# Optimization experiments

Hardware: AMD Instinct MI355X
Metric: run time of the kernel (lower is better)

Reference implementation:

```python
import jax, jax.numpy as jnp
import numpy as np

D_MODEL = 256
HEADS = 4
HEAD_DIM = D_MODEL // HEADS  # 64
BN_EPS = 1e-5


def conv1(x, W, b):
    # Conv1d kernel_size=1 == per-position linear: x [B,C,N], W [O,C], b [O]
    return jnp.einsum('oc,bcn->bon', W, x) + b[:, None]


def setup_inputs() -> dict:
    key = jax.random.key(0)
    ks = jax.random.split(key, 12)
    B, N, M = 4, 4096, 4096
    s = 0.02
    return {
        'x': jax.random.normal(ks[0], (B, D_MODEL, N), jnp.float32),
        'source': jax.random.normal(ks[1], (B, D_MODEL, M), jnp.float32),
        'pq_w': jax.random.normal(ks[2], (D_MODEL, D_MODEL), jnp.float32) * s,
        'pq_b': jnp.zeros((D_MODEL,), jnp.float32),
        'pk_w': jax.random.normal(ks[3], (D_MODEL, D_MODEL), jnp.float32) * s,
        'pk_b': jnp.zeros((D_MODEL,), jnp.float32),
        'pv_w': jax.random.normal(ks[4], (D_MODEL, D_MODEL), jnp.float32) * s,
        'pv_b': jnp.zeros((D_MODEL,), jnp.float32),
        'merge_w': jax.random.normal(ks[5], (D_MODEL, D_MODEL), jnp.float32) * s,
        'merge_b': jnp.zeros((D_MODEL,), jnp.float32),
        'mlp1_w': jax.random.normal(ks[6], (2 * D_MODEL, 2 * D_MODEL), jnp.float32) * s,
        'mlp1_b': jax.random.normal(ks[7], (2 * D_MODEL,), jnp.float32) * s,
        'bn_gamma': jnp.ones((2 * D_MODEL,), jnp.float32),
        'bn_beta': jnp.zeros((2 * D_MODEL,), jnp.float32),
        'mlp2_w': jax.random.normal(ks[8], (D_MODEL, 2 * D_MODEL), jnp.float32) * s,
        'mlp2_b': jnp.zeros((D_MODEL,), jnp.float32),  # nn.init.constant_(mlp[-1].bias, 0.0)
    }


def reference(x, source, pq_w, pq_b, pk_w, pk_b, pv_w, pv_b,
              merge_w, merge_b, mlp1_w, mlp1_b, bn_gamma, bn_beta,
              mlp2_w, mlp2_b):
    B = x.shape[0]
    # projections; torch view(B, dim, heads, -1): channels split as (head_dim, heads)
    q = conv1(x, pq_w, pq_b).reshape(B, HEAD_DIM, HEADS, -1)       # [B,d,h,N]
    k = conv1(source, pk_w, pk_b).reshape(B, HEAD_DIM, HEADS, -1)  # [B,d,h,M]
    v = conv1(source, pv_w, pv_b).reshape(B, HEAD_DIM, HEADS, -1)
    scores = jnp.einsum('bdhn,bdhm->bhnm', q, k) / (HEAD_DIM ** 0.5)
    prob = jax.nn.softmax(scores, axis=-1)                          # [B,h,N,M]
    attn_out = jnp.einsum('bhnm,bdhm->bdhn', prob, v).reshape(B, D_MODEL, -1)
    message = conv1(attn_out, merge_w, merge_b)                     # [B,D,N]
    # MLP: conv(512->512) + BatchNorm1d (training-mode batch stats) + ReLU + conv(512->256)
    h = conv1(jnp.concatenate([x, message], axis=1), mlp1_w, mlp1_b)  # [B,2D,N]
    mean = jnp.mean(h, axis=(0, 2), keepdims=True)
    var = jnp.var(h, axis=(0, 2), keepdims=True)  # biased, as torch BN uses for normalization
    h = bn_gamma[:, None] * (h - mean) * jax.lax.rsqrt(var + BN_EPS) + bn_beta[:, None]
    h = jax.nn.relu(h)
    return conv1(h, mlp2_w, mlp2_b)
```

## Files before the change

kernel.cpp:

```cpp
#include <hip/hip_runtime.h>
#include <hip/hip_bf16.h>

#define D_MODEL 256
#define HEADS 4
#define HD 64
#define BATCH 4
#define SEQ 4096
#define NPOS (BATCH*SEQ)
#define SCALE_LOG2 0.18033688011112042f
#define MCHUNKS 2

typedef __attribute__((ext_vector_type(4))) float floatx4;
typedef __attribute__((ext_vector_type(8))) short bf16x8;
typedef __attribute__((ext_vector_type(4))) short bf16x4;
typedef __attribute__((ext_vector_type(4))) unsigned short ushortx4;

__device__ __forceinline__ float bf2f(unsigned short b) {
    return __uint_as_float(((unsigned int)b) << 16);
}
__device__ __forceinline__ unsigned short f2bf(float f) {
    unsigned int u = __float_as_uint(f);
    return (unsigned short)((u + 0x7fffu + ((u >> 16) & 1u)) >> 16);
}
__device__ __forceinline__ bf16x4 pack_bf16x4(float a, float b, float c, float d) {
    __hip_bfloat162 lo = __float22bfloat162_rn(float2{a, b});
    __hip_bfloat162 hi = __float22bfloat162_rn(float2{c, d});
    union { __hip_bfloat162 h2[2]; bf16x4 v; } u;
    u.h2[0] = lo; u.h2[1] = hi;
    return u.v;
}
__device__ __forceinline__ bf16x8 pack_bf16x8(floatx4 a, floatx4 b) {
    union { bf16x4 h[2]; bf16x8 v; } u;
    u.h[0] = pack_bf16x4(a[0], a[1], a[2], a[3]);
    u.h[1] = pack_bf16x4(b[0], b[1], b[2], b[3]);
    return u.v;
}
#define MFMA(a,b,c) __builtin_amdgcn_mfma_f32_16x16x32_bf16((a),(b),(c),0,0,0)
#define EXP2(x) __builtin_amdgcn_exp2f(x)

__global__ __launch_bounds__(256) void prep_all(
        const float* __restrict__ pq_w, const float* __restrict__ pk_w,
        const float* __restrict__ pv_w, const float* __restrict__ merge_w,
        const float* __restrict__ mlp1_w, const float* __restrict__ mlp2_w,
        const float* __restrict__ mlp1_b, const float* __restrict__ merge_b,
        const float* __restrict__ x, const float* __restrict__ src,
        unsigned short* __restrict__ wqb, unsigned short* __restrict__ wkb,
        unsigned short* __restrict__ wvb,
        unsigned short* __restrict__ w1b, unsigned short* __restrict__ w2b,
        unsigned short* __restrict__ xT, unsigned short* __restrict__ srcT,
        unsigned short* __restrict__ w1f, float* __restrict__ b1f,
        float* __restrict__ bn_zero)
{
    __shared__ unsigned short smem[64 * 264];
    const int t = threadIdx.x;
    const int bx = blockIdx.x;
    if (bx < 576) {
        int linear = bx * 1024 + t * 4;
        const float* srcW; unsigned short* dst; int off;
        if (linear < 65536)       { srcW = pq_w;   dst = wqb; off = 0; }
        else if (linear < 131072) { srcW = pk_w;   dst = wkb; off = 65536; }
        else if (linear < 196608) { srcW = pv_w;   dst = wvb; off = 131072; }
        else if (linear < 458752) { srcW = mlp1_w; dst = w1b; off = 196608; }
        else                      { srcW = mlp2_w; dst = w2b; off = 458752; }
        int i = linear - off;
        float4 w = *(const float4*)&srcW[i];
        ushortx4 s = { f2bf(w.x), f2bf(w.y), f2bf(w.z), f2bf(w.w) };
        *(ushortx4*)&dst[i] = s;
        return;
    }
    if (bx < 1088) {
        unsigned short (*lT)[264] = (unsigned short (*)[264])smem;
        int z = bx - 576;
        const float* X = (z < 256) ? x : src;
        unsigned short* O = (z < 256) ? xT : srcT;
        int rem = z & 255;
        int b = rem >> 6, n0 = (rem & 63) * 64;
#pragma unroll
        for (int r = 0; r < 16; ++r) {
            int idx = r * 256 + t;
            int ch = idx >> 4, nnq = (idx & 15) * 4;
            float4 v4 = *(const float4*)&X[((size_t)b * 256 + ch) * SEQ + n0 + nnq];
            lT[nnq + 0][ch] = f2bf(v4.x);
            lT[nnq + 1][ch] = f2bf(v4.y);
            lT[nnq + 2][ch] = f2bf(v4.z);
            lT[nnq + 3][ch] = f2bf(v4.w);
        }
        __syncthreads();
#pragma unroll
        for (int r = 0; r < 8; ++r) {
            int idx = r * 256 + t;
            int row = idx >> 5, cg = (idx & 31) * 8;
            *(bf16x8*)&O[((size_t)b * SEQ + n0 + row) * 256 + cg] = *(const bf16x8*)&lT[row][cg];
        }
        return;
    }
    if (bx < 1104) {
        unsigned short (*lA)[40] = (unsigned short (*)[40])smem;
        unsigned short (*lB)[40] = (unsigned short (*)[40])(smem + 64 * 40);
        const int lane = t & 63, wid = t >> 6;
        const int wm = wid >> 1, wn = wid & 1;
        const int lrow = lane & 15, quad = lane >> 4;
        const int fb = bx - 1088;
        const int c0  = (fb & 1) * 128;
        const int o20 = (fb >> 1) * 64;

        floatx4 acc[2][4];
#pragma unroll
        for (int i = 0; i < 2; ++i)
#pragma unroll
            for (int j = 0; j < 4; ++j) acc[i][j] = (floatx4){0.f,0.f,0.f,0.f};

        for (int k0 = 0; k0 < 256; k0 += 32) {
#pragma unroll
            for (int r = 0; r < 2; ++r) {
                int linear = r * 1024 + t * 4;
                int row = linear >> 5, col = linear & 31;
                float4 w = *(const float4*)&mlp1_w[(size_t)(o20 + row) * 512 + 256 + k0 + col];
                ushortx4 s = { f2bf(w.x), f2bf(w.y), f2bf(w.z), f2bf(w.w) };
                *(ushortx4*)&lA[row][col] = s;
            }
#pragma unroll
            for (int r = 0; r < 2; ++r) {
                int linear = r * 256 + t;
                int row = linear >> 2, cg = (linear & 3) * 8;
                int cp = c0 + row;
                int pc = ((cp & 63) << 2) | (cp >> 6);
                unsigned short s[8];
#pragma unroll
                for (int j = 0; j < 8; ++j)
                    s[j] = f2bf(merge_w[(size_t)(k0 + cg + j) * 256 + pc]);
                *(bf16x8*)&lB[row][cg] = *(const bf16x8*)s;
            }
            __syncthreads();
            bf16x8 aF[2], bF[4];
            const int kq = quad * 8;
#pragma unroll
            for (int mt = 0; mt < 2; ++mt)
                aF[mt] = *(const bf16x8*)&lA[wm*32 + mt*16 + lrow][kq];
#pragma unroll
            for (int nt = 0; nt < 4; ++nt)
                bF[nt] = *(const bf16x8*)&lB[wn*64 + nt*16 + lrow][kq];
#pragma unroll
            for (int mt = 0; mt < 2; ++mt)
#pragma unroll
                for (int nt = 0; nt < 4; ++nt)
                    acc[mt][nt] = MFMA(aF[mt], bF[nt], acc[mt][nt]);
            __syncthreads();
        }
#pragma unroll
        for (int nt = 0; nt < 4; ++nt) {
            int cp = c0 + wn*64 + nt*16 + lrow;
#pragma unroll
            for (int mt = 0; mt < 2; ++mt)
#pragma unroll
                for (int j = 0; j < 4; ++j) {
                    int o2 = o20 + wm*32 + mt*16 + quad*4 + j;
                    w1f[(size_t)o2 * 256 + cp] = f2bf(acc[mt][nt][j]);
                }
        }
        return;
    }
    if (bx < 1120) {
        int o2 = (bx - 1104) * 32 + (t >> 3);
        int kl = t & 7;
        float s = 0.f;
#pragma unroll
        for (int o = 0; o < 32; ++o)
            s += mlp1_w[(size_t)o2 * 512 + 256 + kl*32 + o] * merge_b[kl*32 + o];
        s += __shfl_xor(s, 1); s += __shfl_xor(s, 2); s += __shfl_xor(s, 4);
        if (kl == 0) b1f[o2] = mlp1_b[o2] + s;
        return;
    }
    *(float4*)&bn_zero[t * 4] = float4{0.f, 0.f, 0.f, 0.f};
}

__global__ __launch_bounds__(256) void proj_qkv_all(
        const unsigned short* __restrict__ Wq, const float* __restrict__ bq,
        const unsigned short* __restrict__ Wk, const float* __restrict__ bk,
        const unsigned short* __restrict__ Wv, const float* __restrict__ bv,
        const unsigned short* __restrict__ xT, const unsigned short* __restrict__ srcT,
        unsigned short* __restrict__ qo, unsigned short* __restrict__ ko,
        unsigned short* __restrict__ vo)
{
    __shared__ unsigned short smem[2][128 * 80];
    unsigned short (*stage)[72] = (unsigned short (*)[72])&smem[0][0];
    unsigned short* stage2 = &smem[0][0];
    const int t = threadIdx.x;
    const int lane = t & 63, wid = t >> 6;
    const int wm = wid >> 1, wn = wid & 1;
    const int lrow = lane & 15, quad = lane >> 4;
    const int mode = blockIdx.x >> 1;
    const int ob = (blockIdx.x & 1) * 128;
    const int n0 = blockIdx.y * 128;
    const int b  = blockIdx.z;
    const unsigned short* W  = (mode == 0) ? Wq : (mode == 1) ? Wk : Wv;
    const float* bias        = (mode == 0) ? bq : (mode == 1) ? bk : bv;
    const unsigned short* XT = (mode == 0) ? xT : srcT;
    unsigned short* out      = (mode == 0) ? qo : (mode == 1) ? ko : vo;

    const int srow[2] = { (0*256 + t) >> 2, (1*256 + t) >> 2 };
    const int scg = (t & 3) * 8;

    floatx4 acc[4][4];
#pragma unroll
    for (int i = 0; i < 4; ++i)
#pragma unroll
        for (int j = 0; j < 4; ++j) acc[i][j] = (floatx4){0.f,0.f,0.f,0.f};

    bf16x8 rW[2], rX[2];
#pragma unroll
    for (int r = 0; r < 2; ++r) {
        rW[r] = *(const bf16x8*)&W[(size_t)(ob + srow[r]) * 256 + scg];
        rX[r] = *(const bf16x8*)&XT[((size_t)b * SEQ + n0 + srow[r]) * 256 + scg];
    }
#pragma unroll
    for (int r = 0; r < 2; ++r) {
        *(bf16x8*)&smem[0][srow[r]*40 + scg]           = rW[r];
        *(bf16x8*)&smem[0][128*40 + srow[r]*40 + scg]  = rX[r];
    }
    __syncthreads();

    int p = 0;
    for (int kc = 0; kc < 8; ++kc) {
        const bool pre = (kc + 1 < 8);
        if (pre) {
            const int k1 = (kc + 1) * 32;
#pragma unroll
            for (int r = 0; r < 2; ++r) {
                rW[r] = *(const bf16x8*)&W[(size_t)(ob + srow[r]) * 256 + k1 + scg];
                rX[r] = *(const bf16x8*)&XT[((size_t)b * SEQ + n0 + srow[r]) * 256 + k1 + scg];
            }
        }
        bf16x8 aF[4], bF[4];
        const int kq = quad * 8;
#pragma unroll
        for (int mt = 0; mt < 4; ++mt)
            aF[mt] = *(const bf16x8*)&smem[p][(wm*64 + mt*16 + lrow)*40 + kq];
#pragma unroll
        for (int nt = 0; nt < 4; ++nt)
            bF[nt] = *(const bf16x8*)&smem[p][128*40 + (wn*64 + nt*16 + lrow)*40 + kq];
#pragma unroll
        for (int mt = 0; mt < 4; ++mt)
#pragma unroll
            for (int nt = 0; nt < 4; ++nt)
                acc[mt][nt] = MFMA(aF[mt], bF[nt], acc[mt][nt]);
        if (pre) {
#pragma unroll
            for (int r = 0; r < 2; ++r) {
                *(bf16x8*)&smem[p^1][srow[r]*40 + scg]          = rW[r];
                *(bf16x8*)&smem[p^1][128*40 + srow[r]*40 + scg] = rX[r];
            }
        }
        __syncthreads();
        p ^= 1;
    }
    const float osc = (mode == 0) ? SCALE_LOG2 : 1.0f;
    if (mode == 2) {
        for (int half = 0; half < 2; ++half) {
            __syncthreads();
            if (wm == half) {
#pragma unroll
                for (int mt = 0; mt < 4; ++mt)
#pragma unroll
                    for (int j = 0; j < 4; ++j) {
                        int ol = mt*16 + quad*4 + j;
                        float bvv = bias[ob + half*64 + ol];
#pragma unroll
                        for (int nt = 0; nt < 4; ++nt) {
                            int n = wn*64 + nt*16 + lrow;
                            stage2[ol*132 + n] = f2bf(acc[mt][nt][j] + bvv);
                        }
                    }
            }
            __syncthreads();
#pragma unroll
            for (int i = 0; i < 4; ++i) {
                int c = i * 256 + t;
                int row = c >> 4, sub = c & 15;
                int o = ob + half*64 + row;
                int d = o >> 2, h = o & 3;
                *(bf16x8*)&out[((size_t)(b*HEADS + h) * HD + d) * SEQ + n0 + sub*8] =
                    *(const bf16x8*)&stage2[row*132 + sub*8];
            }
        }
        return;
    }
    for (int half = 0; half < 2; ++half) {
        __syncthreads();
        if (wm == half) {
#pragma unroll
            for (int mt = 0; mt < 4; ++mt)
#pragma unroll
                for (int j = 0; j < 4; ++j) {
                    int o = ob + half*64 + mt*16 + quad*4 + j;
                    float bvv = bias[o];
                    int col = j*16 + mt*4 + quad;
#pragma unroll
                    for (int nt = 0; nt < 4; ++nt) {
                        int n = wn*64 + nt*16 + lrow;
                        stage[n][col] = f2bf((acc[mt][nt][j] + bvv) * osc);
                    }
                }
        }
        __syncthreads();
#pragma unroll
        for (int i = 0; i < 4; ++i) {
            int c = i * 256 + t;
            int n = c >> 3, h = (c >> 1) & 3, sub = c & 1;
            bf16x8 val = *(const bf16x8*)&stage[n][h*16 + sub*8];
            int d0 = (ob >> 2) + half*16 + sub*8;
            *(bf16x8*)&out[((size_t)(b*HEADS + h) * SEQ + n0 + n) * HD + d0] = val;
        }
    }
}

__global__ __launch_bounds__(256, 2) void flash_attn(
        const unsigned short* __restrict__ q,
        const unsigned short* __restrict__ k,
        const unsigned short* __restrict__ v,
        unsigned short* __restrict__ poO, float* __restrict__ pol)
{
    __shared__ unsigned short smem[2][9216];
    const int t = threadIdx.x, lane = t & 63, wid = t >> 6;
    const int lrow = lane & 15, quad = lane >> 4;
    const int bc = blockIdx.x, qt = blockIdx.y;
    const int bh = bc & 15, chunk = bc >> 4;
    const int hb = (bh & 3) * BATCH + (bh >> 2);
    const int r0 = qt * 256 + wid * 64;

    bf16x8 qf[4][2];
#pragma unroll
    for (int nh = 0; nh < 4; ++nh) {
        const size_t base = ((size_t)bh * SEQ + r0 + nh*16 + lrow) * HD;
        qf[nh][0] = *(const bf16x8*)&q[base + quad * 8];
        qf[nh][1] = *(const bf16x8*)&q[base + 32 + quad * 8];
    }
    bf16x8 ones;
#pragma unroll
    for (int i = 0; i < 8; ++i) ones[i] = (short)0x3F80;
    int mmv[2], cgv[2], krv[2];
#pragma unroll
    for (int r = 0; r < 2; ++r) {
        int linear = r * 256 + t;
        int mm = linear >> 3, cg = (linear & 7) * 8;
        int c2 = mm >> 5, mp = mm & 31;
        mmv[r] = mm; cgv[r] = cg;
        krv[r] = (c2 << 5) + ((mp & 4) << 2) + ((mp >> 3) << 2) + (mp & 3);
    }
    const size_t kbase = ((size_t)bh * SEQ + chunk * (SEQ/MCHUNKS));
    const size_t vbase = (size_t)bh * HD;
    const int moff = chunk * (SEQ/MCHUNKS);
    const int NIT = SEQ / MCHUNKS / 64;

    floatx4 oacc[4][4], oaccL[4];
#pragma unroll
    for (int nh = 0; nh < 4; ++nh) {
        oaccL[nh] = (floatx4){0.f,0.f,0.f,0.f};
#pragma unroll
        for (int i = 0; i < 4; ++i) oacc[nh][i] = (floatx4){0.f,0.f,0.f,0.f};
    }

    {
        bf16x8 pk[2], pv[2];
#pragma unroll
        for (int r = 0; r < 2; ++r) {
            pk[r] = *(const bf16x8*)&k[(kbase + mmv[r]) * HD + cgv[r]];
            pv[r] = *(const bf16x8*)&v[(vbase + mmv[r]) * SEQ + moff + cgv[r]];
        }
#pragma unroll
        for (int r = 0; r < 2; ++r) {
            *(bf16x8*)&smem[0][krv[r]*72 + cgv[r]]        = pk[r];
            *(bf16x8*)&smem[0][4608 + mmv[r]*72 + cgv[r]] = pv[r];
        }
    }
    __syncthreads();

    int p = 0;
#pragma unroll 1
    for (int it = 0; it < NIT; ++it) {
        bf16x8 pk[2], pv[2];
        const bool pre = (it + 1 < NIT);
        if (pre) {
            const int m1 = (it + 1) * 64;
#pragma unroll
            for (int r = 0; r < 2; ++r) {
                pk[r] = *(const bf16x8*)&k[(kbase + m1 + mmv[r]) * HD + cgv[r]];
                pv[r] = *(const bf16x8*)&v[(vbase + mmv[r]) * SEQ + moff + m1 + cgv[r]];
            }
        }
        const unsigned short* lS = smem[p];

#pragma unroll
        for (int c2 = 0; c2 < 2; ++c2) {
            floatx4 sa[2][4];
#pragma unroll
            for (int AB = 0; AB < 2; ++AB)
#pragma unroll
                for (int nh = 0; nh < 4; ++nh)
                    sa[AB][nh] = (floatx4){0.f,0.f,0.f,0.f};
            __builtin_amdgcn_s_setprio(1);
#pragma unroll
            for (int AB = 0; AB < 2; ++AB) {
#pragma unroll
                for (int kc = 0; kc < 2; ++kc) {
                    bf16x8 kf = *(const bf16x8*)&lS[(c2*32 + AB*16 + lrow)*72 + kc*32 + quad*8];
#pragma unroll
                    for (int nh = 0; nh < 4; ++nh)
                        sa[AB][nh] = MFMA(kf, qf[nh][kc], sa[AB][nh]);
                }
            }
            __builtin_amdgcn_s_setprio(0);
            bf16x8 pf8[4];
#pragma unroll
            for (int nh = 0; nh < 4; ++nh) {
                floatx4 ea, eb;
#pragma unroll
                for (int i = 0; i < 4; ++i) { ea[i] = EXP2(sa[0][nh][i]); eb[i] = EXP2(sa[1][nh][i]); }
                pf8[nh] = pack_bf16x8(ea, eb);
            }
            __builtin_amdgcn_s_setprio(1);
#pragma unroll
            for (int nh = 0; nh < 4; ++nh)
                oaccL[nh] = MFMA(ones, pf8[nh], oaccL[nh]);
#pragma unroll
            for (int dt = 0; dt < 4; ++dt) {
                bf16x8 vf = *(const bf16x8*)&lS[4608 + (dt*16 + lrow)*72 + c2*32 + quad*8];
#pragma unroll
                for (int nh = 0; nh < 4; ++nh)
                    oacc[nh][dt] = MFMA(vf, pf8[nh], oacc[nh][dt]);
            }
            __builtin_amdgcn_s_setprio(0);
        }
        if (pre) {
#pragma unroll
            for (int r = 0; r < 2; ++r) {
                *(bf16x8*)&smem[p^1][krv[r]*72 + cgv[r]]        = pk[r];
                *(bf16x8*)&smem[p^1][4608 + mmv[r]*72 + cgv[r]] = pv[r];
            }
        }
        __syncthreads();
        p ^= 1;
    }
    const size_t nb = (size_t)hb * SEQ + qt * 256;
    if (lane < 16) {
#pragma unroll
        for (int nh = 0; nh < 4; ++nh)
            pol[(nb + wid*64 + nh*16 + lrow) * MCHUNKS + chunk] = oaccL[nh][0];
    }
    unsigned short* stB = (unsigned short*)&smem[0][0];
#pragma unroll
    for (int nh = 0; nh < 4; ++nh)
#pragma unroll
        for (int dt = 0; dt < 4; ++dt) {
            bf16x4 pv4 = pack_bf16x4(oacc[nh][dt][0], oacc[nh][dt][1],
                                     oacc[nh][dt][2], oacc[nh][dt][3]);
            *(bf16x4*)&stB[(wid*64 + nh*16 + lrow)*72 + dt*16 + quad*4] = pv4;
        }
    __syncthreads();
#pragma unroll
    for (int i = 0; i < 8; ++i) {
        int c = i * 256 + t;
        int row = c >> 3, sub = c & 7;
        *(bf16x8*)&poO[((nb + row) * MCHUNKS + chunk) * HD + sub*8] =
            *(const bf16x8*)&stB[row*72 + sub*8];
    }
}

__global__ __launch_bounds__(512) void gemm_mlp1(
        const unsigned short* __restrict__ xT, const unsigned short* __restrict__ poO,
        const float* __restrict__ pol,
        const unsigned short* __restrict__ w1b, const unsigned short* __restrict__ w1f,
        const float* __restrict__ b1f, unsigned short* __restrict__ h1,
        float* __restrict__ sums, float* __restrict__ sumsq)
{
    __shared__ unsigned short lA[2][128][40];
    __shared__ unsigned short lB[2][256][40];
    __shared__ float sInv[512];
    __shared__ float sRed[4][4][16][2];
    const int t = threadIdx.x;
    const int lane = t & 63, wid = t >> 6;
    const int wp = wid >> 2, wo = wid & 3;
    const int lrow = lane & 15, quad = lane >> 4;
    const int o0 = blockIdx.x * 256;
    const int p0 = blockIdx.y * 128;
    const int b = p0 >> 12, n0 = p0 & (SEQ - 1);

    {
        int h = t >> 7, nn = t & 127;
        int hb = h * BATCH + b;
        float2 l2 = *(const float2*)&pol[((size_t)hb * SEQ + n0 + nn) * MCHUNKS];
        sInv[t] = 1.0f / (l2.x + l2.y);
    }
    __syncthreads();

    const int arow = t >> 2, acg = (t & 3) * 8;
    const int brow[2] = { (0*512 + t) >> 2, (1*512 + t) >> 2 };

    floatx4 acc[4][4];
#pragma unroll
    for (int i = 0; i < 4; ++i)
#pragma unroll
        for (int j = 0; j < 4; ++j) acc[i][j] = (floatx4){0.f,0.f,0.f,0.f};

    auto loadT = [&](int k0, bf16x8& ra, bf16x8& rb, bf16x8 (&rBv)[2]) {
        if (k0 < 256) {
            ra = *(const bf16x8*)&xT[(size_t)(p0 + arow) * 256 + k0 + acg];
#pragma unroll
            for (int r = 0; r < 2; ++r)
                rBv[r] = *(const bf16x8*)&w1b[(size_t)(o0 + brow[r]) * 512 + k0 + acg];
        } else {
            const int kk2 = k0 - 256;
            const int h = kk2 >> 6, d0 = kk2 & 63, hb = h * BATCH + b;
            const unsigned short* bse =
                &poO[(((size_t)hb * SEQ + n0 + arow) * MCHUNKS) * HD + d0 + acg];
            ra = *(const bf16x8*)bse;
            rb = *(const bf16x8*)(bse + HD);
#pragma unroll
            for (int r = 0; r < 2; ++r)
                rBv[r] = *(const bf16x8*)&w1f[(size_t)(o0 + brow[r]) * 256 + kk2 + acg];
        }
    };
    auto storeT = [&](int buf, int k0, bf16x8& ra, bf16x8& rb, bf16x8 (&rBv)[2]) {
        bf16x8 av;
        if (k0 < 256) {
            av = ra;
        } else {
            const int kk2 = k0 - 256;
            const int h = kk2 >> 6;
            float inv = sInv[h*128 + arow];
            unsigned short res[8];
#pragma unroll
            for (int i = 0; i < 8; ++i)
                res[i] = f2bf((bf2f((unsigned short)ra[i]) + bf2f((unsigned short)rb[i])) * inv);
            av = *(const bf16x8*)res;
        }
        *(bf16x8*)&lA[buf][arow][acg] = av;
#pragma unroll
        for (int r = 0; r < 2; ++r) *(bf16x8*)&lB[buf][brow[r]][acg] = rBv[r];
    };
    auto computeT = [&](int buf) {
        bf16x8 aF[4], bF[4];
        const int kq = quad * 8;
#pragma unroll
        for (int mt = 0; mt < 4; ++mt)
            aF[mt] = *(const bf16x8*)&lA[buf][wp*64 + mt*16 + lrow][kq];
#pragma unroll
        for (int nt = 0; nt < 4; ++nt)
            bF[nt] = *(const bf16x8*)&lB[buf][wo*64 + nt*16 + lrow][kq];
#pragma unroll
        for (int mt = 0; mt < 4; ++mt)
#pragma unroll
            for (int nt = 0; nt < 4; ++nt)
                acc[mt][nt] = MFMA(aF[mt], bF[nt], acc[mt][nt]);
    };

    bf16x8 rAa0, rAb0, rB0[2];
    bf16x8 rAa1, rAb1, rB1[2];

    loadT(0, rAa0, rAb0, rB0);
    storeT(0, 0, rAa0, rAb0, rB0);
    loadT(32, rAa0, rAb0, rB0);
    __syncthreads();

#pragma unroll
    for (int kc = 0; kc < 16; kc += 2) {
        if (kc + 2 < 16) loadT((kc + 2) * 32, rAa1, rAb1, rB1);
        computeT(0);
        storeT(1, (kc + 1) * 32, rAa0, rAb0, rB0);
        __syncthreads();
        if (kc + 3 < 16) loadT((kc + 3) * 32, rAa0, rAb0, rB0);
        computeT(1);
        if (kc + 2 < 16) storeT(0, (kc + 2) * 32, rAa1, rAb1, rB1);
        __syncthreads();
    }
#pragma unroll
    for (int nt = 0; nt < 4; ++nt) {
        int o = o0 + wo*64 + nt*16 + lrow;
        float bvv = b1f[o];
        float s = 0.f, qs = 0.f;
#pragma unroll
        for (int mt = 0; mt < 4; ++mt)
#pragma unroll
            for (int j = 0; j < 4; ++j) {
                int pos = p0 + wp*64 + mt*16 + quad*4 + j;
                float val = acc[mt][nt][j] + bvv;
                h1[(size_t)pos * 512 + o] = f2bf(val);
                s += val; qs += val * val;
            }
        s  += __shfl_xor(s, 16);  s  += __shfl_xor(s, 32);
        qs += __shfl_xor(qs, 16); qs += __shfl_xor(qs, 32);
        if (wp == 1 && lane < 16) {
            sRed[wo][nt][lrow][0] = s;
            sRed[wo][nt][lrow][1] = qs;
        }
        __syncthreads();
        if (wp == 0 && lane < 16) {
            atomicAdd(&sums[o],  s  + sRed[wo][nt][lrow][0]);
            atomicAdd(&sumsq[o], qs + sRed[wo][nt][lrow][1]);
        }
    }
}

__global__ __launch_bounds__(256) void gemm_mlp2(
        const unsigned short* __restrict__ W2, const unsigned short* __restrict__ h1,
        const float* __restrict__ bias,
        const float* __restrict__ sums, const float* __restrict__ sumsq,
        const float* __restrict__ gamma, const float* __restrict__ beta,
        float* __restrict__ out)
{
    __shared__ unsigned short lA[2][128][40];
    __shared__ unsigned short lB[2][64][40];
    __shared__ float sSc[512], sSh[512];
    const int t = threadIdx.x;
    const int lane = t & 63, wid = t >> 6;
    const int wm = wid >> 1, wn = wid & 1;
    const int lrow = lane & 15, quad = lane >> 4;
    const int o0 = blockIdx.x * 128;
    const int p0 = blockIdx.y * 64;

#pragma unroll
    for (int cc = 0; cc < 2; ++cc) {
        int c = cc * 256 + t;
        float mean = sums[c] * (1.0f / NPOS);
        float var  = sumsq[c] * (1.0f / NPOS) - mean * mean;
        float sc = gamma[c] * rsqrtf(var + 1e-5f);
        sSc[c] = sc;
        sSh[c] = beta[c] - mean * sc;
    }
    __syncthreads();

    const int arow[2] = { (0*256 + t) >> 2, (1*256 + t) >> 2 };
    const int acg = (t & 3) * 8;
    const int brow = t >> 2;

    floatx4 acc[4][2];
#pragma unroll
    for (int i = 0; i < 4; ++i)
#pragma unroll
        for (int j = 0; j < 2; ++j) acc[i][j] = (floatx4){0.f,0.f,0.f,0.f};

    auto loadT = [&](int k0, bf16x8 (&rw)[2], bf16x8& rh) {
#pragma unroll
        for (int r = 0; r < 2; ++r)
            rw[r] = *(const bf16x8*)&W2[(size_t)(o0 + arow[r]) * 512 + k0 + acg];
        rh = *(const bf16x8*)&h1[(size_t)(p0 + brow) * 512 + k0 + acg];
    };
    auto storeT = [&](int buf, int k0, bf16x8 (&rw)[2], bf16x8& rh) {
#pragma unroll
        for (int r = 0; r < 2; ++r) *(bf16x8*)&lA[buf][arow[r]][acg] = rw[r];
        unsigned short res[8];
#pragma unroll
        for (int i = 0; i < 8; ++i) {
            int c = k0 + acg + i;
            float f = bf2f((unsigned short)rh[i]);
            f = fmaxf(f * sSc[c] + sSh[c], 0.f);
            res[i] = f2bf(f);
        }
        *(bf16x8*)&lB[buf][brow][acg] = *(const bf16x8*)res;
    };
    auto computeT = [&](int buf) {
        bf16x8 aF[4], bF[2];
        const int kq = quad * 8;
#pragma unroll
        for (int mt = 0; mt < 4; ++mt)
            aF[mt] = *(const bf16x8*)&lA[buf][wm*64 + mt*16 + lrow][kq];
#pragma unroll
        for (int nt = 0; nt < 2; ++nt)
            bF[nt] = *(const bf16x8*)&lB[buf][wn*32 + nt*16 + lrow][kq];
#pragma unroll
        for (int mt = 0; mt < 4; ++mt)
#pragma unroll
            for (int nt = 0; nt < 2; ++nt)
                acc[mt][nt] = MFMA(aF[mt], bF[nt], acc[mt][nt]);
    };

    bf16x8 rW0[2], rH0, rW1[2], rH1;

    loadT(0, rW0, rH0);
    storeT(0, 0, rW0, rH0);
    loadT(32, rW0, rH0);
    __syncthreads();

#pragma unroll
    for (int kc = 0; kc < 16; kc += 2) {
        if (kc + 2 < 16) loadT((kc + 2) * 32, rW1, rH1);
        computeT(0);
        storeT(1, (kc + 1) * 32, rW0, rH0);
        __syncthreads();
        if (kc + 3 < 16) loadT((kc + 3) * 32, rW0, rH0);
        computeT(1);
        if (kc + 2 < 16) storeT(0, (kc + 2) * 32, rW1, rH1);
        __syncthreads();
    }
#pragma unroll
    for (int mt = 0; mt < 4; ++mt)
#pragma unroll
        for (int j = 0; j < 4; ++j) {
            int o = o0 + wm*64 + mt*16 + quad*4 + j;
            float bvv = bias[o];
#pragma unroll
            for (int nt = 0; nt < 2; ++nt) {
                int pos = p0 + wn*32 + nt*16 + lrow;
                int b = pos >> 12, n = pos & (SEQ - 1);
                out[((size_t)b * D_MODEL + o) * SEQ + n] = acc[mt][nt][j] + bvv;
            }
        }
}

extern "C" void kernel_launch(void* const* d_in, const int* in_sizes, int n_in,
                              void* d_out, int out_size, void* d_ws, size_t ws_size,
                              hipStream_t stream)
{
    (void)in_sizes; (void)n_in; (void)out_size; (void)ws_size;
    const float* x        = (const float*)d_in[0];
    const float* source   = (const float*)d_in[1];
    const float* pq_w     = (const float*)d_in[2];
    const float* pq_b     = (const float*)d_in[3];
    const float* pk_w     = (const float*)d_in[4];
    const float* pk_b     = (const float*)d_in[5];
    const float* pv_w     = (const float*)d_in[6];
    const float* pv_b     = (const float*)d_in[7];
    const float* merge_w  = (const float*)d_in[8];
    const float* merge_b  = (const float*)d_in[9];
    const float* mlp1_w   = (const float*)d_in[10];
    const float* mlp1_b   = (const float*)d_in[11];
    const float* bn_gamma = (const float*)d_in[12];
    const float* bn_beta  = (const float*)d_in[13];
    const float* mlp2_w   = (const float*)d_in[14];
    const float* mlp2_b   = (const float*)d_in[15];
    float* out = (float*)d_out;

    char* ws = (char*)d_ws;
    const size_t MB = 1ull << 20;
    unsigned short* xT   = (unsigned short*)(ws);
    unsigned short* srcT = (unsigned short*)(ws + 8*MB);
    unsigned short* q    = (unsigned short*)(ws + 16*MB);
    unsigned short* kk   = (unsigned short*)(ws + 24*MB);
    unsigned short* v    = (unsigned short*)(ws + 32*MB);
    unsigned short* poO  = (unsigned short*)(ws + 40*MB);
    unsigned short* h1   = (unsigned short*)(ws + 16*MB);
    float* pol = (float*)(ws + 72*MB);
    unsigned short* wqb = (unsigned short*)(ws + 73*MB);
    unsigned short* wkb = wqb + 65536;
    unsigned short* wvb = wkb + 65536;
    unsigned short* w1b = wvb + 65536;
    unsigned short* w2b = w1b + 262144;
    unsigned short* w1f = w2b + 131072;
    float* b1f = (float*)(w1f + 131072);
    float* bn_sum = b1f + 512;
    float* bn_sumsq = bn_sum + 512;

    prep_all<<<dim3(1121), 256, 0, stream>>>(
        pq_w, pk_w, pv_w, merge_w, mlp1_w, mlp2_w, mlp1_b, merge_b, x, source,
        wqb, wkb, wvb, w1b, w2b, xT, srcT, w1f, b1f, bn_sum);
    proj_qkv_all<<<dim3(6, SEQ/128, BATCH), 256, 0, stream>>>(
        wqb, pq_b, wkb, pk_b, wvb, pv_b, xT, srcT, q, kk, v);
    flash_attn<<<dim3(16*MCHUNKS, SEQ/256), 256, 0, stream>>>(q, kk, v, poO, pol);
    gemm_mlp1<<<dim3(2, NPOS/128), 512, 0, stream>>>(
        xT, poO, pol, w1b, w1f, b1f, h1, bn_sum, bn_sumsq);
    gemm_mlp2<<<dim3(2, NPOS/64), 256, 0, stream>>>(
        w2b, h1, mlp2_b, bn_sum, bn_sumsq, bn_gamma, bn_beta, out);
}
```

Measured before the change: 231.7 us.

## Load V fragments directly from global into registers, halve flash-attn LDS

```diff
diff --git a/kernel.cpp b/kernel.cpp
--- a/kernel.cpp
+++ b/kernel.cpp
@@ -320,7 +320,7 @@
         const unsigned short* __restrict__ v,
         unsigned short* __restrict__ poO, float* __restrict__ pol)
 {
-    __shared__ unsigned short smem[2][9216];
+    __shared__ unsigned short smem[2][4608];
     const int t = threadIdx.x, lane = t & 63, wid = t >> 6;
     const int lrow = lane & 15, quad = lane >> 4;
     const int bc = blockIdx.x, qt = blockIdx.y;
@@ -348,9 +348,9 @@
         krv[r] = (c2 << 5) + ((mp & 4) << 2) + ((mp >> 3) << 2) + (mp & 3);
     }
     const size_t kbase = ((size_t)bh * SEQ + chunk * (SEQ/MCHUNKS));
-    const size_t vbase = (size_t)bh * HD;
     const int moff = chunk * (SEQ/MCHUNKS);
     const int NIT = SEQ / MCHUNKS / 64;
+    const unsigned short* vrow = &v[((size_t)bh * HD + lrow) * SEQ + moff + quad * 8];
 
     floatx4 oacc[4][4], oaccL[4];
 #pragma unroll
@@ -361,34 +361,36 @@
     }
 
     {
-        bf16x8 pk[2], pv[2];
-#pragma unroll
-        for (int r = 0; r < 2; ++r) {
+        bf16x8 pk[2];
+#pragma unroll
+        for (int r = 0; r < 2; ++r)
             pk[r] = *(const bf16x8*)&k[(kbase + mmv[r]) * HD + cgv[r]];
-            pv[r] = *(const bf16x8*)&v[(vbase + mmv[r]) * SEQ + moff + cgv[r]];
-        }
-#pragma unroll
-        for (int r = 0; r < 2; ++r) {
-            *(bf16x8*)&smem[0][krv[r]*72 + cgv[r]]        = pk[r];
-            *(bf16x8*)&smem[0][4608 + mmv[r]*72 + cgv[r]] = pv[r];
-        }
+#pragma unroll
+        for (int r = 0; r < 2; ++r)
+            *(bf16x8*)&smem[0][krv[r]*72 + cgv[r]] = pk[r];
     }
     __syncthreads();
 
     int p = 0;
 #pragma unroll 1
     for (int it = 0; it < NIT; ++it) {
-        bf16x8 pk[2], pv[2];
+        bf16x8 pk[2];
         const bool pre = (it + 1 < NIT);
         if (pre) {
             const int m1 = (it + 1) * 64;
 #pragma unroll
-            for (int r = 0; r < 2; ++r) {
+            for (int r = 0; r < 2; ++r)
                 pk[r] = *(const bf16x8*)&k[(kbase + m1 + mmv[r]) * HD + cgv[r]];
-                pv[r] = *(const bf16x8*)&v[(vbase + mmv[r]) * SEQ + moff + m1 + cgv[r]];
-            }
         }
         const unsigned short* lS = smem[p];
+        const int mit = it * 64;
+
+        bf16x8 vfr[2][4];
+#pragma unroll
+        for (int c2 = 0; c2 < 2; ++c2)
+#pragma unroll
+            for (int dt = 0; dt < 4; ++dt)
+                vfr[c2][dt] = *(const bf16x8*)&vrow[(size_t)dt * 16 * SEQ + mit + c2*32];
 
 #pragma unroll
         for (int c2 = 0; c2 < 2; ++c2) {
@@ -424,19 +426,16 @@
                 oaccL[nh] = MFMA(ones, pf8[nh], oaccL[nh]);
 #pragma unroll
             for (int dt = 0; dt < 4; ++dt) {
-                bf16x8 vf = *(const bf16x8*)&lS[4608 + (dt*16 + lrow)*72 + c2*32 + quad*8];
 #pragma unroll
                 for (int nh = 0; nh < 4; ++nh)
-                    oacc[nh][dt] = MFMA(vf, pf8[nh], oacc[nh][dt]);
+                    oacc[nh][dt] = MFMA(vfr[c2][dt], pf8[nh], oacc[nh][dt]);
             }
             __builtin_amdgcn_s_setprio(0);
         }
         if (pre) {
 #pragma unroll
-            for (int r = 0; r < 2; ++r) {
-                *(bf16x8*)&smem[p^1][krv[r]*72 + cgv[r]]        = pk[r];
-                *(bf16x8*)&smem[p^1][4608 + mmv[r]*72 + cgv[r]] = pv[r];
-            }
+            for (int r = 0; r < 2; ++r)
+                *(bf16x8*)&smem[p^1][krv[r]*72 + cgv[r]] = pk[r];
         }
         __syncthreads();
         p ^= 1;
@@ -449,20 +448,27 @@
     }
     unsigned short* stB = (unsigned short*)&smem[0][0];
 #pragma unroll
-    for (int nh = 0; nh < 4; ++nh)
-#pragma unroll
-        for (int dt = 0; dt < 4; ++dt) {
-            bf16x4 pv4 = pack_bf16x4(oacc[nh][dt][0], oacc[nh][dt][1],
-                                     oacc[nh][dt][2], oacc[nh][dt][3]);
-            *(bf16x4*)&stB[(wid*64 + nh*16 + lrow)*72 + dt*16 + quad*4] = pv4;
-        }
-    __syncthreads();
-#pragma unroll
-    for (int i = 0; i < 8; ++i) {
-        int c = i * 256 + t;
-        int row = c >> 3, sub = c & 7;
-        *(bf16x8*)&poO[((nb + row) * MCHUNKS + chunk) * HD + sub*8] =
-            *(const bf16x8*)&stB[row*72 + sub*8];
+    for (int hp = 0; hp < 2; ++hp) {
+        if ((wid >> 1) == hp) {
+#pragma unroll
+            for (int nh = 0; nh < 4; ++nh)
+#pragma unroll
+                for (int dt = 0; dt < 4; ++dt) {
+                    bf16x4 pv4 = pack_bf16x4(oacc[nh][dt][0], oacc[nh][dt][1],
+                                             oacc[nh][dt][2], oacc[nh][dt][3]);
+                    int lr = (wid & 1)*64 + nh*16 + lrow;
+                    *(bf16x4*)&stB[lr*72 + dt*16 + quad*4] = pv4;
+                }
+        }
+        __syncthreads();
+#pragma unroll
+        for (int i = 0; i < 4; ++i) {
+            int c = i * 256 + t;
+            int row = c >> 3, sub = c & 7;
+            *(bf16x8*)&poO[((nb + hp*128 + row) * MCHUNKS + chunk) * HD + sub*8] =
+                *(const bf16x8*)&stB[row*72 + sub*8];
+        }
+        __syncthreads();
     }
 }
 
```

Result: slower. 243.6 us (+5.1%).
